# Kernel optimization log

Measured on AMD Instinct MI355X. Metric: run time of the kernel, lower is better.

Reference implementation:

```python
import jax, jax.numpy as jnp
import numpy as np

D_MODEL, N_EXPERTS, N_VIEWS, N_TOKENS = 256, 16, 3, 8192

def setup_inputs() -> dict:
    key = jax.random.key(0)
    ks = jax.random.split(key, 10)
    s = 0.05
    return {
        "v0": jax.random.normal(ks[0], (N_TOKENS, D_MODEL), jnp.float32),
        "v1": jax.random.normal(ks[1], (N_TOKENS, D_MODEL), jnp.float32),
        "v2": jax.random.normal(ks[2], (N_TOKENS, D_MODEL), jnp.float32),
        "router_w": jax.random.normal(ks[3], (N_VIEWS, N_EXPERTS, D_MODEL), jnp.float32) * s,
        "expert_keys": jax.random.normal(ks[4], (N_EXPERTS, D_MODEL), jnp.float32) * s,
        "W1": jax.random.normal(ks[5], (N_EXPERTS, D_MODEL, 4 * D_MODEL), jnp.float32) * s,
        "b1": jax.random.normal(ks[6], (N_EXPERTS, 4 * D_MODEL), jnp.float32) * s,
        "W2": jax.random.normal(ks[7], (N_EXPERTS, 4 * D_MODEL, D_MODEL), jnp.float32) * s,
        "b2": jax.random.normal(ks[8], (N_EXPERTS, D_MODEL), jnp.float32) * s,
        "top_k": 4,
    }

def _laplace_gate(v, rw, expert_keys, top_k):
    # -||v - key||^2 expanded: -(|v|^2 + |k|^2 - 2 v.k)   -> [N, E]
    sq = (jnp.sum(v * v, -1, keepdims=True)
          + jnp.sum(expert_keys * expert_keys, -1)[None, :]
          - 2.0 * (v @ expert_keys.T))
    logits = -sq + v @ rw.T                      # router(h), no bias
    topv, topi = jax.lax.top_k(logits, top_k)    # [N, K]
    gate = jax.nn.softmax(topv, axis=-1)         # exp(topv - logsumexp(topv))
    return gate, topi

def reference(v0, v1, v2, router_w, expert_keys, W1, b1, W2, b2, top_k):
    views = [v0, v1, v2]
    E = expert_keys.shape[0]
    N = v0.shape[0]
    fused = jnp.zeros_like(v0)
    rows = jnp.arange(N)[:, None]
    for i, v in enumerate(views):
        gate, idx = _laplace_gate(v, router_w[i], expert_keys, top_k)
        # scatter top-k gates into a dense [N, E] combine matrix
        dense_gate = jnp.zeros((N, E), v.dtype).at[rows, idx].add(gate)
        out = jnp.zeros_like(v)
        for e in range(E):  # fixed small expert loop; each token combined via its gate
            h = jax.nn.gelu(v @ W1[e] + b1[e], approximate=False)
            out = out + dense_gate[:, e:e + 1] * (h @ W2[e] + b2[e])
        fused = fused + out
    return fused
```

## Files before the change

kernel.cpp:

```cpp
#include <hip/hip_runtime.h>
#include <math.h>

#define D_MODEL 256
#define N_EXP   16
#define N_VIEWS 3
#define N_TOK   8192
#define TOPK    4
#define HDIM    1024
#define CH      64
#define NCH     16
#define ROWS    64
#define NGROUP  48
#define NT_STRIPE 2048
#define NT_SPILL  512
#define NT_TOTAL  (NT_STRIPE + NT_SPILL)
#define REC_ELTS 32768

typedef short s16x8 __attribute__((ext_vector_type(8)));
typedef float f32x4 __attribute__((ext_vector_type(4)));

__device__ __forceinline__ unsigned short f2bf(float x) {
    union { float f; unsigned u; } a; a.f = x;
    unsigned r = a.u + 0x7FFFu + ((a.u >> 16) & 1u);
    return (unsigned short)(r >> 16);
}

__device__ __forceinline__ void dma16(const unsigned short* gp, unsigned short* lp) {
    __builtin_amdgcn_global_load_lds(
        (const __attribute__((address_space(1))) unsigned int*)gp,
        (__attribute__((address_space(3))) unsigned int*)lp, 16, 0, 0);
}

__device__ __forceinline__ void dma_half(const unsigned short* gsrc, unsigned short* ldst,
                                         int wave, int lane) {
    #pragma unroll
    for (int i = 0; i < 4; i++) {
        int blk = wave * 4 + i;
        dma16(gsrc + ((size_t)blk * 64 + lane) * 8, ldst + blk * 512);
    }
}

#define T1_STRIDE 65
#define T2_STRIDE 257

__global__ __launch_bounds__(256) void prep_kernel(
    const float* __restrict__ v0, const float* __restrict__ v1, const float* __restrict__ v2,
    const float* __restrict__ rw, const float* __restrict__ keys,
    const float* __restrict__ W1, const float* __restrict__ W2,
    unsigned short* __restrict__ Wf, unsigned short* __restrict__ Xbf,
    int* __restrict__ gidx, float* __restrict__ ggate, int* __restrict__ counts)
{
    __shared__ __align__(16) char smem[256 * T1_STRIDE * 4];

    int bid = blockIdx.x;
    int tid = threadIdx.x;
    if (bid < 512) {
        int c = bid & 15, e = (bid >> 4) & 15, z = bid >> 8;
        unsigned short* dst = Wf + (size_t)(e * NCH + c) * REC_ELTS;
        if (z == 0) {
            float* T1 = (float*)smem;
            const float* src = W1 + (size_t)e * 256 * 1024 + c * 64;
            #pragma unroll
            for (int p = 0; p < 16; p++) {
                int k = p * 16 + (tid >> 4), c4 = (tid & 15) * 4;
                float4 v = *(const float4*)(src + (size_t)k * 1024 + c4);
                T1[k * T1_STRIDE + c4]     = v.x;
                T1[k * T1_STRIDE + c4 + 1] = v.y;
                T1[k * T1_STRIDE + c4 + 2] = v.z;
                T1[k * T1_STRIDE + c4 + 3] = v.w;
            }
            __syncthreads();
            #pragma unroll
            for (int i = 0; i < 8; i++) {
                int idx = tid + i * 256;
                int lane = idx & 63, nt = (idx >> 6) & 3, ks = idx >> 8;
                int nl = nt * 16 + (lane & 15);
                int kbase = ks * 32 + (lane >> 4) * 8;
                s16x8 o;
                #pragma unroll
                for (int j = 0; j < 8; j++) o[j] = (short)f2bf(T1[(kbase + j) * T1_STRIDE + nl]);
                *(s16x8*)(dst + (size_t)idx * 8) = o;
            }
        } else {
            float* T2 = (float*)smem;
            const float* src = W2 + ((size_t)e * 1024 + c * 64) * 256;
            #pragma unroll
            for (int p = 0; p < 16; p++) {
                int k2l = p * 4 + (tid >> 6), c4 = (tid & 63) * 4;
                float4 v = *(const float4*)(src + (size_t)k2l * 256 + c4);
                T2[k2l * T2_STRIDE + c4]     = v.x;
                T2[k2l * T2_STRIDE + c4 + 1] = v.y;
                T2[k2l * T2_STRIDE + c4 + 2] = v.z;
                T2[k2l * T2_STRIDE + c4 + 3] = v.w;
            }
            __syncthreads();
            dst += 16384;
            #pragma unroll
            for (int i = 0; i < 8; i++) {
                int idx = tid + i * 256;
                int lane = idx & 63, ntile = (idx >> 6) & 15, ks2 = idx >> 10;
                int n = ntile * 16 + (lane & 15);
                int kbase = ks2 * 32 + (lane >> 4) * 8;
                s16x8 o;
                #pragma unroll
                for (int j = 0; j < 8; j++) o[j] = (short)f2bf(T2[(kbase + j) * T2_STRIDE + n]);
                *(s16x8*)(dst + (size_t)idx * 8) = o;
            }
        }
        return;
    }

    float* cwS = (float*)smem;
    float* knS = (float*)(smem + 16384);
    int*  lcnt = (int*)(smem + 16384 + 64);
    int rb = bid - 512;
    int view = rb >> 7, xb = rb & 127;
    const float* src = view == 0 ? v0 : (view == 1 ? v1 : v2);
    for (int i = tid; i < N_EXP * D_MODEL; i += 256)
        cwS[i] = rw[view * N_EXP * D_MODEL + i] + 2.0f * keys[i];
    if (tid < N_EXP) {
        const float4* kp = (const float4*)(keys + tid * D_MODEL);
        float s = 0.f;
        for (int d = 0; d < 64; d++) { float4 k = kp[d]; s += k.x*k.x + k.y*k.y + k.z*k.z + k.w*k.w; }
        knS[tid] = s; lcnt[tid] = 0;
    }
    __syncthreads();

    int wave = tid >> 6, lane = tid & 63;
    for (int t = 0; t < 16; t++) {
        int token = xb * 64 + wave * 16 + t;
        float4 v = ((const float4*)(src + (size_t)token * D_MODEL))[lane];
        ushort4 xo; xo.x = f2bf(v.x); xo.y = f2bf(v.y); xo.z = f2bf(v.z); xo.w = f2bf(v.w);
        ((ushort4*)(Xbf + ((size_t)view * N_TOK + token) * D_MODEL))[lane] = xo;
        float lg[N_EXP];
        #pragma unroll
        for (int e = 0; e < N_EXP; e++) {
            float4 w = *(const float4*)&cwS[e * D_MODEL + lane * 4];
            float p = v.x * w.x + v.y * w.y + v.z * w.z + v.w * w.w;
            #pragma unroll
            for (int s = 32; s > 0; s >>= 1) p += __shfl_xor(p, s, 64);
            lg[e] = p - knS[e];
        }
        int idxs[TOPK]; float vals[TOPK];
        #pragma unroll
        for (int k = 0; k < TOPK; k++) {
            float best = -1e30f; int bi = 0;
            #pragma unroll
            for (int e = 0; e < N_EXP; e++)
                if (lg[e] > best) { best = lg[e]; bi = e; }
            idxs[k] = bi; vals[k] = best;
            #pragma unroll
            for (int e = 0; e < N_EXP; e++)
                lg[e] = (e == bi) ? -1e30f : lg[e];
        }
        float m = vals[0], s = 0.f, ex[TOPK];
        #pragma unroll
        for (int k = 0; k < TOPK; k++) { ex[k] = __expf(vals[k] - m); s += ex[k]; }
        float inv = 1.0f / s;
        if (lane == 0) {
            size_t t4 = ((size_t)view * N_TOK + token) * TOPK;
            int4 gi; gi.x = idxs[0]; gi.y = idxs[1]; gi.z = idxs[2]; gi.w = idxs[3];
            *(int4*)&gidx[t4] = gi;
            float4 gv; gv.x = ex[0]*inv; gv.y = ex[1]*inv; gv.z = ex[2]*inv; gv.w = ex[3]*inv;
            *(float4*)&ggate[t4] = gv;
            atomicAdd(&lcnt[idxs[0]], 1); atomicAdd(&lcnt[idxs[1]], 1);
            atomicAdd(&lcnt[idxs[2]], 1); atomicAdd(&lcnt[idxs[3]], 1);
        }
    }
    __syncthreads();
    if (tid < N_EXP && lcnt[tid])
        atomicAdd(&counts[view * N_EXP + tid], lcnt[tid]);
}

__global__ void scan_kernel(const int* __restrict__ counts, int* __restrict__ offs,
                            int* __restrict__ cursor, int* __restrict__ tiles,
                            int* __restrict__ spillCnt) {
    __shared__ int ntS[NGROUP];
    int t = threadIdx.x;
    if (t == 0) spillCnt[0] = 0;
    if (t < NGROUP) ntS[t] = (counts[t] + ROWS - 1) / ROWS;
    for (int s = t; s < NT_TOTAL; s += 64) tiles[s] = -1;
    __syncthreads();
    if (t <= NGROUP) {
        int acc = 0;
        for (int g = 0; g < t && g < NGROUP; g++) acc += counts[g];
        if (t < NGROUP) { offs[t] = acc; cursor[t] = acc; }
        else offs[NGROUP] = acc;
    }
    if (t < NGROUP) {
        int x = (t & 15) >> 1;
        int kstart = 0;
        for (int g2 = 0; g2 < t; g2++)
            if (((g2 & 15) >> 1) == x) kstart += ntS[g2];
        int nt = ntS[t];
        for (int i = 0; i < nt; i++) {
            int k = kstart + i, rec = (t << 16) | i;
            if (k < NT_STRIPE / 8) tiles[x + 8 * k] = rec;
            else {
                int sp = atomicAdd(spillCnt, 1);
                if (sp < NT_SPILL) tiles[NT_STRIPE + sp] = rec;
            }
        }
    }
}

__global__ __launch_bounds__(256) void fill_kernel(const int* __restrict__ gidx,
                                                   const float* __restrict__ ggate,
                                                   int* __restrict__ cursor,
                                                   int* __restrict__ rowTok,
                                                   float* __restrict__ rowGate) {
    __shared__ int lc[N_EXP], lbase[N_EXP];
    int view = blockIdx.y;
    int token = blockIdx.x * 256 + threadIdx.x;
    if (threadIdx.x < N_EXP) lc[threadIdx.x] = 0;
    __syncthreads();
    size_t t4 = ((size_t)view * N_TOK + token) * TOPK;
    int4 e4 = *(const int4*)&gidx[t4];
    float4 g4 = *(const float4*)&ggate[t4];
    int e[4] = { e4.x, e4.y, e4.z, e4.w };
    float gg[4] = { g4.x, g4.y, g4.z, g4.w };
    int lp[4];
    #pragma unroll
    for (int k = 0; k < TOPK; k++) lp[k] = atomicAdd(&lc[e[k]], 1);
    __syncthreads();
    if (threadIdx.x < N_EXP)
        lbase[threadIdx.x] = lc[threadIdx.x] ? atomicAdd(&cursor[view * N_EXP + threadIdx.x], lc[threadIdx.x]) : 0;
    __syncthreads();
    #pragma unroll
    for (int k = 0; k < TOPK; k++) {
        int pos = lbase[e[k]] + lp[k];
        rowTok[pos] = token;
        rowGate[pos] = gg[k];
    }
}

__global__ __launch_bounds__(512, 4) void ffn_kernel(
    const unsigned short* __restrict__ Xbf, const unsigned short* __restrict__ Wf,
    const float* __restrict__ b1, const float* __restrict__ b2,
    const int* __restrict__ offs, const int* __restrict__ tiles,
    const int* __restrict__ rowTok, const float* __restrict__ rowGate,
    float* __restrict__ out)
{
    __shared__ __align__(16) unsigned short Wbuf[REC_ELTS];
    __shared__ __align__(16) unsigned short Hc[ROWS * CH];
    __shared__ int   tokS[ROWS];
    __shared__ float gateS[ROWS];

    int rec = tiles[blockIdx.x];
    if (rec < 0) return;
    int g = rec >> 16, view = g >> 4, e = g & 15;
    int base = offs[g];
    int L = offs[g + 1] - base;
    int r0 = (rec & 0xffff) * ROWS;

    int tid = threadIdx.x;
    int wave = tid >> 6, lane = tid & 63, lmod = lane & 15, quad = lane >> 4;

    const unsigned short* wchunk = Wf + (size_t)e * NCH * REC_ELTS;
    dma_half(wchunk, Wbuf, wave, lane);

    if (tid < ROWS) {
        int gr = r0 + tid; bool ok = gr < L;
        tokS[tid]  = ok ? rowTok[base + gr] : -1;
        gateS[tid] = ok ? rowGate[base + gr] : 0.f;
    }

    int mt1 = wave & 3, nh = wave >> 2;
    int ms  = wave & 1, ns = wave >> 1;

    __syncthreads();

    s16x8 areg[8];
    {
        int token = tokS[mt1 * 16 + lmod];
        if (token < 0) token = 0;
        const unsigned short* xp = Xbf + ((size_t)view * N_TOK + token) * D_MODEL;
        #pragma unroll
        for (int ks = 0; ks < 8; ks++)
            areg[ks] = *(const s16x8*)(xp + ks * 32 + quad * 8);
    }
    dma_half(wchunk + 16384, Wbuf + 16384, wave, lane);

    f32x4 acc2[2][4];
    #pragma unroll
    for (int i = 0; i < 2; i++)
        #pragma unroll
        for (int j = 0; j < 4; j++) acc2[i][j] = (f32x4){0.f, 0.f, 0.f, 0.f};

    for (int c = 0; c < NCH; c++) {
        f32x4 acc1[2];
        acc1[0] = (f32x4){0.f, 0.f, 0.f, 0.f};
        acc1[1] = (f32x4){0.f, 0.f, 0.f, 0.f};
        #pragma unroll
        for (int ks = 0; ks < 8; ks++) {
            #pragma unroll
            for (int nt = 0; nt < 2; nt++) {
                s16x8 b = *(const s16x8*)&Wbuf[((ks * 4 + nh * 2 + nt) * 64 + lane) * 8];
                acc1[nt] = __builtin_amdgcn_mfma_f32_16x16x32_bf16(areg[ks], b, acc1[nt], 0, 0, 0);
            }
        }
        #pragma unroll
        for (int nt = 0; nt < 2; nt++) {
            float bb = b1[e * HDIM + c * CH + (nh * 2 + nt) * 16 + lmod];
            int qa = nt * 2 + (lmod >> 3);
            int baseo = ((mt1 * 2 + nh) * 64 + qa * 16 + quad * 4) * 8 + (lmod & 7);
            #pragma unroll
            for (int r = 0; r < 4; r++) {
                float h = acc1[nt][r] + bb;
                float u = h * (0.7978845608f + 0.0356774081f * h * h);
                float ex2 = __expf(2.f * u);
                float tn = 1.f - 2.f * __builtin_amdgcn_rcpf(1.f + ex2);
                Hc[baseo + r * 8] = f2bf(0.5f * h * (1.f + tn));
            }
        }
        __syncthreads();
        if (c < NCH - 1)
            dma_half(wchunk + (size_t)(c + 1) * REC_ELTS, Wbuf, wave, lane);
        #pragma unroll
        for (int ks2 = 0; ks2 < 2; ks2++) {
            s16x8 afr[2];
            #pragma unroll
            for (int mt = 0; mt < 2; mt++)
                afr[mt] = *(const s16x8*)&Hc[(((ms * 2 + mt) * 2 + ks2) * 64 + lane) * 8];
            #pragma unroll
            for (int nt = 0; nt < 4; nt++) {
                s16x8 b = *(const s16x8*)&Wbuf[16384 + ((ks2 * 16 + ns * 4 + nt) * 64 + lane) * 8];
                #pragma unroll
                for (int mt = 0; mt < 2; mt++)
                    acc2[mt][nt] = __builtin_amdgcn_mfma_f32_16x16x32_bf16(
                        afr[mt], b, acc2[mt][nt], 0, 0, 0);
            }
        }
        __syncthreads();
        if (c < NCH - 1)
            dma_half(wchunk + (size_t)(c + 1) * REC_ELTS + 16384, Wbuf + 16384, wave, lane);
    }

    #pragma unroll
    for (int nt = 0; nt < 4; nt++) {
        int col = (ns * 4 + nt) * 16 + lmod;
        float b2v = b2[e * D_MODEL + col];
        #pragma unroll
        for (int mt = 0; mt < 2; mt++) {
            #pragma unroll
            for (int r = 0; r < 4; r++) {
                int rloc = (ms * 2 + mt) * 16 + quad * 4 + r;
                if (r0 + rloc < L) {
                    atomicAdd(&out[(size_t)tokS[rloc] * D_MODEL + col],
                              gateS[rloc] * (acc2[mt][nt][r] + b2v));
                }
            }
        }
    }
}

extern "C" void kernel_launch(void* const* d_in, const int* in_sizes, int n_in,
                              void* d_out, int out_size, void* d_ws, size_t ws_size,
                              hipStream_t stream)
{
    const float* v0   = (const float*)d_in[0];
    const float* v1   = (const float*)d_in[1];
    const float* v2   = (const float*)d_in[2];
    const float* rw   = (const float*)d_in[3];
    const float* keys = (const float*)d_in[4];
    const float* W1   = (const float*)d_in[5];
    const float* b1   = (const float*)d_in[6];
    const float* W2   = (const float*)d_in[7];
    const float* b2   = (const float*)d_in[8];
    float* out = (float*)d_out;

    char* p = (char*)d_ws;
    unsigned short* Xbf = (unsigned short*)p; p += (size_t)N_VIEWS * N_TOK * D_MODEL * 2;
    unsigned short* Wf  = (unsigned short*)p; p += (size_t)N_EXP * NCH * REC_ELTS * 2;
    int*   counts = (int*)p;   p += 256;
    int*   offs   = (int*)p;   p += 256;
    int*   cursor = (int*)p;   p += 256;
    int*   spill  = (int*)p;   p += 256;
    int*   tiles  = (int*)p;   p += NT_TOTAL * 4 + 64;
    int*   gidx   = (int*)p;   p += (size_t)N_VIEWS * N_TOK * TOPK * 4;
    float* ggate  = (float*)p; p += (size_t)N_VIEWS * N_TOK * TOPK * 4;
    int*   rowTok = (int*)p;   p += (size_t)N_VIEWS * N_TOK * TOPK * 4;
    float* rowGate= (float*)p; p += (size_t)N_VIEWS * N_TOK * TOPK * 4;

    hipMemsetAsync(counts, 0, NGROUP * sizeof(int), stream);
    hipMemsetAsync(out, 0, (size_t)out_size * sizeof(float), stream);

    prep_kernel<<<896, 256, 0, stream>>>(v0, v1, v2, rw, keys, W1, W2,
                                         Wf, Xbf, gidx, ggate, counts);
    scan_kernel<<<1, 64, 0, stream>>>(counts, offs, cursor, tiles, spill);
    fill_kernel<<<dim3(N_TOK / 256, N_VIEWS), 256, 0, stream>>>(gidx, ggate, cursor,
                                                                rowTok, rowGate);
    ffn_kernel<<<dim3(NT_TOTAL), 512, 0, stream>>>(Xbf, Wf, b1, b2, offs, tiles,
                                                   rowTok, rowGate, out);
}
```

Before: 391.5 us.

## Fuse routing scatter into prep kernel, drop scan/fill kernels with fixed-capacity groups

The prep kernel now reserves per-expert slots with a global atomicAdd and writes token/gate rows straight into fixed-capacity per-(view,expert) buckets. This removes the separate scan and fill kernels and the gidx/ggate intermediate buffers. The FFN grid becomes a static 6144-block enumeration mapped by XCD, and blocks whose tile index exceeds the group count exit early. The aim is to cut two kernel launches and their global round-trips, at the cost of many empty early-exit blocks and a serial 256-iteration scan run by 16 threads per prep block.

```diff
diff --git a/kernel.cpp b/kernel.cpp
--- a/kernel.cpp
+++ b/kernel.cpp
@@ -11,9 +11,7 @@
 #define NCH     16
 #define ROWS    64
 #define NGROUP  48
-#define NT_STRIPE 2048
-#define NT_SPILL  512
-#define NT_TOTAL  (NT_STRIPE + NT_SPILL)
+#define GCAP    8192
 #define REC_ELTS 32768
 
 typedef short s16x8 __attribute__((ext_vector_type(8)));
@@ -48,7 +46,7 @@
     const float* __restrict__ rw, const float* __restrict__ keys,
     const float* __restrict__ W1, const float* __restrict__ W2,
     unsigned short* __restrict__ Wf, unsigned short* __restrict__ Xbf,
-    int* __restrict__ gidx, float* __restrict__ ggate, int* __restrict__ counts)
+    int* __restrict__ counts, int* __restrict__ rowTok, float* __restrict__ rowGate)
 {
     __shared__ __align__(16) char smem[256 * T1_STRIDE * 4];
 
@@ -110,9 +108,13 @@
         return;
     }
 
-    float* cwS = (float*)smem;
-    float* knS = (float*)(smem + 16384);
-    int*  lcnt = (int*)(smem + 16384 + 64);
+    float* cwS  = (float*)smem;
+    float* knS  = (float*)(smem + 16384);
+    int*   lcnt = (int*)(smem + 16448);
+    int*   eIdx = (int*)(smem + 16512);
+    float* gV   = (float*)(smem + 17536);
+    int*  lbase = (int*)(smem + 18560);
+
     int rb = bid - 512;
     int view = rb >> 7, xb = rb & 127;
     const float* src = view == 0 ? v0 : (view == 1 ? v1 : v2);
@@ -128,7 +130,8 @@
 
     int wave = tid >> 6, lane = tid & 63;
     for (int t = 0; t < 16; t++) {
-        int token = xb * 64 + wave * 16 + t;
+        int tl = wave * 16 + t;
+        int token = xb * 64 + tl;
         float4 v = ((const float4*)(src + (size_t)token * D_MODEL))[lane];
         ushort4 xo; xo.x = f2bf(v.x); xo.y = f2bf(v.y); xo.z = f2bf(v.z); xo.w = f2bf(v.w);
         ((ushort4*)(Xbf + ((size_t)view * N_TOK + token) * D_MODEL))[lane] = xo;
@@ -158,100 +161,52 @@
         for (int k = 0; k < TOPK; k++) { ex[k] = __expf(vals[k] - m); s += ex[k]; }
         float inv = 1.0f / s;
         if (lane == 0) {
-            size_t t4 = ((size_t)view * N_TOK + token) * TOPK;
-            int4 gi; gi.x = idxs[0]; gi.y = idxs[1]; gi.z = idxs[2]; gi.w = idxs[3];
-            *(int4*)&gidx[t4] = gi;
-            float4 gv; gv.x = ex[0]*inv; gv.y = ex[1]*inv; gv.z = ex[2]*inv; gv.w = ex[3]*inv;
-            *(float4*)&ggate[t4] = gv;
-            atomicAdd(&lcnt[idxs[0]], 1); atomicAdd(&lcnt[idxs[1]], 1);
-            atomicAdd(&lcnt[idxs[2]], 1); atomicAdd(&lcnt[idxs[3]], 1);
+            #pragma unroll
+            for (int k = 0; k < TOPK; k++) {
+                eIdx[tl * 4 + k] = idxs[k];
+                gV[tl * 4 + k] = ex[k] * inv;
+                atomicAdd(&lcnt[idxs[k]], 1);
+            }
         }
     }
     __syncthreads();
-    if (tid < N_EXP && lcnt[tid])
-        atomicAdd(&counts[view * N_EXP + tid], lcnt[tid]);
-}
-
-__global__ void scan_kernel(const int* __restrict__ counts, int* __restrict__ offs,
-                            int* __restrict__ cursor, int* __restrict__ tiles,
-                            int* __restrict__ spillCnt) {
-    __shared__ int ntS[NGROUP];
-    int t = threadIdx.x;
-    if (t == 0) spillCnt[0] = 0;
-    if (t < NGROUP) ntS[t] = (counts[t] + ROWS - 1) / ROWS;
-    for (int s = t; s < NT_TOTAL; s += 64) tiles[s] = -1;
+    if (tid < N_EXP)
+        lbase[tid] = lcnt[tid] ? atomicAdd(&counts[view * N_EXP + tid], lcnt[tid]) : 0;
     __syncthreads();
-    if (t <= NGROUP) {
-        int acc = 0;
-        for (int g = 0; g < t && g < NGROUP; g++) acc += counts[g];
-        if (t < NGROUP) { offs[t] = acc; cursor[t] = acc; }
-        else offs[NGROUP] = acc;
-    }
-    if (t < NGROUP) {
-        int x = (t & 15) >> 1;
-        int kstart = 0;
-        for (int g2 = 0; g2 < t; g2++)
-            if (((g2 & 15) >> 1) == x) kstart += ntS[g2];
-        int nt = ntS[t];
-        for (int i = 0; i < nt; i++) {
-            int k = kstart + i, rec = (t << 16) | i;
-            if (k < NT_STRIPE / 8) tiles[x + 8 * k] = rec;
-            else {
-                int sp = atomicAdd(spillCnt, 1);
-                if (sp < NT_SPILL) tiles[NT_STRIPE + sp] = rec;
-            }
-        }
-    }
-}
-
-__global__ __launch_bounds__(256) void fill_kernel(const int* __restrict__ gidx,
-                                                   const float* __restrict__ ggate,
-                                                   int* __restrict__ cursor,
-                                                   int* __restrict__ rowTok,
-                                                   float* __restrict__ rowGate) {
-    __shared__ int lc[N_EXP], lbase[N_EXP];
-    int view = blockIdx.y;
-    int token = blockIdx.x * 256 + threadIdx.x;
-    if (threadIdx.x < N_EXP) lc[threadIdx.x] = 0;
-    __syncthreads();
-    size_t t4 = ((size_t)view * N_TOK + token) * TOPK;
-    int4 e4 = *(const int4*)&gidx[t4];
-    float4 g4 = *(const float4*)&ggate[t4];
-    int e[4] = { e4.x, e4.y, e4.z, e4.w };
-    float gg[4] = { g4.x, g4.y, g4.z, g4.w };
-    int lp[4];
-    #pragma unroll
-    for (int k = 0; k < TOPK; k++) lp[k] = atomicAdd(&lc[e[k]], 1);
-    __syncthreads();
-    if (threadIdx.x < N_EXP)
-        lbase[threadIdx.x] = lc[threadIdx.x] ? atomicAdd(&cursor[view * N_EXP + threadIdx.x], lc[threadIdx.x]) : 0;
-    __syncthreads();
-    #pragma unroll
-    for (int k = 0; k < TOPK; k++) {
-        int pos = lbase[e[k]] + lp[k];
-        rowTok[pos] = token;
-        rowGate[pos] = gg[k];
+    if (tid < N_EXP) {
+        int e = tid;
+        int dstbase = (view * N_EXP + e) * GCAP + lbase[e];
+        int c = 0;
+        for (int i = 0; i < 256; i++) {
+            if (eIdx[i] == e) {
+                rowTok[dstbase + c]  = xb * 64 + (i >> 2);
+                rowGate[dstbase + c] = gV[i];
+                c++;
+            }
+        }
     }
 }
 
 __global__ __launch_bounds__(512, 4) void ffn_kernel(
     const unsigned short* __restrict__ Xbf, const unsigned short* __restrict__ Wf,
     const float* __restrict__ b1, const float* __restrict__ b2,
-    const int* __restrict__ offs, const int* __restrict__ tiles,
-    const int* __restrict__ rowTok, const float* __restrict__ rowGate,
-    float* __restrict__ out)
+    const int* __restrict__ counts, const int* __restrict__ rowTok,
+    const float* __restrict__ rowGate, float* __restrict__ out)
 {
     __shared__ __align__(16) unsigned short Wbuf[REC_ELTS];
     __shared__ __align__(16) unsigned short Hc[ROWS * CH];
     __shared__ int   tokS[ROWS];
     __shared__ float gateS[ROWS];
 
-    int rec = tiles[blockIdx.x];
-    if (rec < 0) return;
-    int g = rec >> 16, view = g >> 4, e = g & 15;
-    int base = offs[g];
-    int L = offs[g + 1] - base;
-    int r0 = (rec & 0xffff) * ROWS;
+    int s = blockIdx.x;
+    int xcd = s & 7, k = s >> 3;
+    int j = k % 6, ti = k / 6;
+    int e = 2 * xcd + (j & 1), view = j >> 1;
+    int g = view * N_EXP + e;
+    int L = counts[g];
+    int r0 = ti * ROWS;
+    if (r0 >= L) return;
+    int base = g * GCAP;
 
     int tid = threadIdx.x;
     int wave = tid >> 6, lane = tid & 63, lmod = lane & 15, quad = lane >> 4;
@@ -285,7 +240,7 @@
     #pragma unroll
     for (int i = 0; i < 2; i++)
         #pragma unroll
-        for (int j = 0; j < 4; j++) acc2[i][j] = (f32x4){0.f, 0.f, 0.f, 0.f};
+        for (int jj = 0; jj < 4; jj++) acc2[i][jj] = (f32x4){0.f, 0.f, 0.f, 0.f};
 
     for (int c = 0; c < NCH; c++) {
         f32x4 acc1[2];
@@ -373,23 +328,14 @@
     unsigned short* Xbf = (unsigned short*)p; p += (size_t)N_VIEWS * N_TOK * D_MODEL * 2;
     unsigned short* Wf  = (unsigned short*)p; p += (size_t)N_EXP * NCH * REC_ELTS * 2;
     int*   counts = (int*)p;   p += 256;
-    int*   offs   = (int*)p;   p += 256;
-    int*   cursor = (int*)p;   p += 256;
-    int*   spill  = (int*)p;   p += 256;
-    int*   tiles  = (int*)p;   p += NT_TOTAL * 4 + 64;
-    int*   gidx   = (int*)p;   p += (size_t)N_VIEWS * N_TOK * TOPK * 4;
-    float* ggate  = (float*)p; p += (size_t)N_VIEWS * N_TOK * TOPK * 4;
-    int*   rowTok = (int*)p;   p += (size_t)N_VIEWS * N_TOK * TOPK * 4;
-    float* rowGate= (float*)p; p += (size_t)N_VIEWS * N_TOK * TOPK * 4;
+    int*   rowTok = (int*)p;   p += (size_t)NGROUP * GCAP * 4;
+    float* rowGate= (float*)p; p += (size_t)NGROUP * GCAP * 4;
 
     hipMemsetAsync(counts, 0, NGROUP * sizeof(int), stream);
     hipMemsetAsync(out, 0, (size_t)out_size * sizeof(float), stream);
 
     prep_kernel<<<896, 256, 0, stream>>>(v0, v1, v2, rw, keys, W1, W2,
-                                         Wf, Xbf, gidx, ggate, counts);
-    scan_kernel<<<1, 64, 0, stream>>>(counts, offs, cursor, tiles, spill);
-    fill_kernel<<<dim3(N_TOK / 256, N_VIEWS), 256, 0, stream>>>(gidx, ggate, cursor,
-                                                                rowTok, rowGate);
-    ffn_kernel<<<dim3(NT_TOTAL), 512, 0, stream>>>(Xbf, Wf, b1, b2, offs, tiles,
-                                                   rowTok, rowGate, out);
-}
+                                         Wf, Xbf, counts, rowTok, rowGate);
+    ffn_kernel<<<8 * 768, 512, 0, stream>>>(Xbf, Wf, b1, b2, counts,
+                                            rowTok, rowGate, out);
+}
```

Result: slower. 403.2 us (+3.0%).
